# Kernel tuning notes

Measured on AMD Instinct MI355X. Metric: run time of the kernel, lower is better.

The kernel has to match this reference:

```python
import jax, jax.numpy as jnp
import numpy as np

B, NH, T, N, D = 4, 8, 2048, 512, 128
THETA = 2.0 ** 16
GAMMA = 0.995


def setup_inputs() -> dict:
    key = jax.random.key(0)
    kq, kv, ks = jax.random.split(key, 3)
    Q = jax.random.normal(kq, (B, NH, T, N), jnp.float32)
    V = jax.random.normal(kv, (B, NH, T, D), jnp.float32)
    S_prev = 0.01 * jax.random.normal(ks, (B, NH, N, D), jnp.float32)
    # get_freqs(N, theta=2**16): per-channel inverse frequencies
    freqs = jnp.asarray(1.0 / THETA ** (np.arange(N, dtype=np.float32) / N), jnp.float32)
    gamma = jnp.float32(GAMMA)
    return {"Q": Q, "V": V, "S_prev": S_prev, "freqs": freqs, "gamma": gamma}


def _rope(phases, v):
    """Rotary embedding with per-channel phases. phases broadcasts against v's
    last two dims (T, N); rotate-half formulation."""
    cos, sin = jnp.cos(phases), jnp.sin(phases)
    half = v.shape[-1] // 2
    v_rot = jnp.concatenate([-v[..., half:], v[..., :half]], axis=-1)
    return v * cos + v_rot * sin


def reference(Q, V, S_prev, freqs, gamma):
    # Q: (B,nh,T,N)  V: (B,nh,T,D)  S_prev: (B,nh,N,D)
    t_len = Q.shape[2]
    phases = jnp.arange(t_len, dtype=freqs.dtype)[:, None] * freqs[None, :]  # (T,N)
    QR = _rope(phases[None, None], Q)  # K == Q per the module's assert

    q_seq = jnp.moveaxis(QR, 2, 0)  # (T,B,nh,N)
    v_seq = jnp.moveaxis(V, 2, 0)   # (T,B,nh,D)

    def step(S, qv):
        q_t, v_t = qv
        out_t = jnp.einsum('bhn,bhnd->bhd', q_t, S)          # read before write
        S_new = (S + jnp.einsum('bhn,bhd->bhnd', q_t, v_t)) * gamma  # write + decay
        return S_new, out_t

    S_final, outs = jax.lax.scan(step, S_prev, (q_seq, v_seq))
    output = jnp.moveaxis(outs, 0, 2)  # (B,nh,T,D)
    return output, S_final
```

## Files before the change

kernel.cpp:

```cpp
#include <hip/hip_runtime.h>
#include <hip/hip_bf16.h>

typedef __attribute__((ext_vector_type(8))) short short8;
typedef __attribute__((ext_vector_type(4))) short short4v;
typedef __attribute__((ext_vector_type(4))) float f32x4;

#define MFMA16(a,b,c) __builtin_amdgcn_mfma_f32_16x16x32_bf16((a),(b),(c),0,0,0)

constexpr int BHn = 32;
constexpr int Tn  = 2048;
constexpr int Nn  = 512;
constexpr int Dn  = 128;
constexpr int CHn = 64;
constexpr int NCH = Tn / CHn;

static __device__ __forceinline__ unsigned short f2b(float x){
  __hip_bfloat16 h = __float2bfloat16(x);
  return *reinterpret_cast<unsigned short*>(&h);
}

__global__ __launch_bounds__(256) void rope_k(const float* __restrict__ Q,
                                              const float* __restrict__ freqs,
                                              unsigned short* __restrict__ QRq){
  int tq  = blockIdx.x & 511;
  int bh0 = (blockIdx.x >> 9) << 3;
  int np  = threadIdx.x;
  float f1 = freqs[np], f2 = freqs[np + 256];
  float s1[4], c1[4], s2[4], c2[4];
  #pragma unroll
  for (int i = 0; i < 4; ++i){
    float tf = (float)(tq * 4 + i);
    sincosf(tf * f1, &s1[i], &c1[i]);
    sincosf(tf * f2, &s2[i], &c2[i]);
  }
  for (int b = 0; b < 8; ++b){
    int bh = bh0 + b;
    const float* qp = Q + (size_t)bh * Tn * Nn + (size_t)(tq * 4) * Nn + np;
    short4v o1, o2;
    #pragma unroll
    for (int i = 0; i < 4; ++i){
      float q1 = qp[(size_t)i * Nn], q2 = qp[(size_t)i * Nn + 256];
      o1[i] = (short)f2b(q1 * c1[i] - q2 * s1[i]);
      o2[i] = (short)f2b(q2 * c2[i] + q1 * s2[i]);
    }
    unsigned short* dst = QRq + (size_t)bh * Tn * Nn + (size_t)tq * 2048;
    *reinterpret_cast<short4v*>(dst + np * 4)         = o1;
    *reinterpret_cast<short4v*>(dst + (np + 256) * 4) = o2;
  }
}

__device__ __forceinline__ short8 ldfrag(const unsigned short* buf, int rowbase, int k0, int ld, int lane){
  int row = rowbase + (lane & 15);
  int col = (k0 + ((lane >> 4) << 3)) ^ ((row & 7) << 3);
  return *reinterpret_cast<const short8*>(buf + row * ld + col);
}

__device__ __forceinline__ void stage_q(unsigned short* Rs, uint4 v, int dt0, int n0){
  unsigned w0 = v.x, w1 = v.y, w2 = v.z, w3 = v.w;
  unsigned o0 = (w0 & 0xffffu) | (w2 << 16);
  unsigned o1 = (w0 >> 16)     | (w2 & 0xffff0000u);
  unsigned o2 = (w1 & 0xffffu) | (w3 << 16);
  unsigned o3 = (w1 >> 16)     | (w3 & 0xffff0000u);
  *reinterpret_cast<unsigned*>(&Rs[(dt0    ) * 512 + (n0 ^ (((dt0    ) & 7) << 3))]) = o0;
  *reinterpret_cast<unsigned*>(&Rs[(dt0 + 1) * 512 + (n0 ^ (((dt0 + 1) & 7) << 3))]) = o1;
  *reinterpret_cast<unsigned*>(&Rs[(dt0 + 2) * 512 + (n0 ^ (((dt0 + 2) & 7) << 3))]) = o2;
  *reinterpret_cast<unsigned*>(&Rs[(dt0 + 3) * 512 + (n0 ^ (((dt0 + 3) & 7) << 3))]) = o3;
}

__global__ __launch_bounds__(512, 1) void lattn_main(
    const unsigned short* __restrict__ QRq,
    const float* __restrict__ V,
    const float* __restrict__ S_prev,
    const float* __restrict__ gammap,
    float* __restrict__ Out,
    float* __restrict__ Sfin)
{
  __shared__ __align__(16) unsigned short Rs [64 * 512];
  __shared__ __align__(16) unsigned short SbTs[16 * 512];
  __shared__ __align__(16) unsigned short VTs[2][16 * 64];
  __shared__ __align__(16) unsigned short Ps [64 * 64];
  __shared__ float gpow[65], gpinv[65];

  const int tid  = threadIdx.x;
  const int w    = tid >> 6;
  const int lane = tid & 63;
  const int bh   = blockIdx.x & 31;
  const int dch  = blockIdx.x >> 5;
  const int d0   = dch * 16;
  const float g  = gammap[0];

  const unsigned short* QRbh = QRq + (size_t)bh * Tn * Nn;
  const float* Vbh = V + (size_t)bh * Tn * Dn;

  if (tid < 65){
    gpow[tid]  = powf(g,  (float)tid);
    gpinv[tid] = powf(g, -(float)tid);
  }
  #pragma unroll
  for (int i = tid; i < 64 * 64; i += 512) Ps[i] = 0;

  f32x4 st[8];
  if (w >= 4){
    int r0 = (w - 4) * 8;
    #pragma unroll
    for (int j = 0; j < 8; ++j){
      int n = (r0 + j) * 16 + (lane & 15);
      const float* sp = S_prev + (size_t)bh * Nn * Dn + (size_t)n * Dn + d0 + ((lane >> 4) << 2);
      st[j] = *reinterpret_cast<const f32x4*>(sp);
    }
  }
  __syncthreads();
  const float g64 = gpow[64];

  {
    #pragma unroll
    for (int i = 0; i < 8; ++i){
      int p = tid + i * 512;
      int tql = p >> 8, n0 = (p & 255) << 1;
      uint4 v = *reinterpret_cast<const uint4*>(QRbh + (size_t)tql * 2048 + n0 * 4);
      stage_q(Rs, v, tql << 2, n0);
    }
    {
      int dtv = tid >> 3, dp = (tid & 7) << 1;
      const float* vp = Vbh + (size_t)dtv * Dn + d0 + dp;
      float sc = gpinv[dtv];
      VTs[0][ dp      * 64 + (dtv ^ (( dp      & 7) << 3))] = f2b(vp[0] * sc);
      VTs[0][(dp + 1) * 64 + (dtv ^ (((dp + 1) & 7) << 3))] = f2b(vp[1] * sc);
    }
    if (w >= 4){
      int r0 = (w - 4) * 8;
      #pragma unroll
      for (int j = 0; j < 8; ++j){
        int n  = (r0 + j) * 16 + (lane & 15);
        int dl = (lane >> 4) << 2;
        #pragma unroll
        for (int r = 0; r < 4; ++r){
          int d = dl + r;
          SbTs[d * 512 + (n ^ ((d & 7) << 3))] = f2b(st[j][r]);
        }
      }
    }
  }
  __syncthreads();

  for (int c = 0; c < NCH; ++c){
    const int t0 = c * CHn;
    const int vb = c & 1;
    const bool pf = (c + 1 < NCH);
    const unsigned short* Qc = QRbh + (size_t)t0 * Nn;

    uint4 rq[8];
    float va0 = 0.f, va1 = 0.f;
    const int dtv_ = tid >> 3;
    if (pf){
      const unsigned short* QRc = QRbh + (size_t)(t0 + CHn) * Nn;
      #pragma unroll
      for (int i = 0; i < 8; ++i){
        int p = tid + i * 512;
        int tql = p >> 8, n0 = (p & 255) << 1;
        rq[i] = *reinterpret_cast<const uint4*>(QRc + (size_t)tql * 2048 + n0 * 4);
      }
      const float* vp = Vbh + (size_t)(t0 + CHn + dtv_) * Dn + d0 + ((tid & 7) << 1);
      va0 = vp[0]; va1 = vp[1];
    }

    f32x4 oacc = {0.f, 0.f, 0.f, 0.f};
    if (w < 4){
      f32x4 p0 = {0.f,0.f,0.f,0.f}, p1 = p0, p2 = p0;
      for (int kb = 0; kb < 16; ++kb){
        int k0 = kb * 32;
        short8 fs = ldfrag(SbTs, 0, k0, 512, lane);
        if (w == 0){
          short8 f0 = ldfrag(Rs,  0, k0, 512, lane);
          short8 f1 = ldfrag(Rs, 16, k0, 512, lane);
          p0   = MFMA16(f0, f0, p0);
          p1   = MFMA16(f1, f0, p1);
          p2   = MFMA16(f1, f1, p2);
          oacc = MFMA16(fs, f0, oacc);
        } else if (w == 1){
          short8 f0 = ldfrag(Rs,  0, k0, 512, lane);
          short8 f1 = ldfrag(Rs, 16, k0, 512, lane);
          short8 f2 = ldfrag(Rs, 32, k0, 512, lane);
          p0   = MFMA16(f2, f0, p0);
          p1   = MFMA16(f2, f1, p1);
          p2   = MFMA16(f2, f2, p2);
          oacc = MFMA16(fs, f2, oacc);
        } else if (w == 2){
          short8 f0 = ldfrag(Rs,  0, k0, 512, lane);
          short8 f1 = ldfrag(Rs, 16, k0, 512, lane);
          short8 f3 = ldfrag(Rs, 48, k0, 512, lane);
          p0   = MFMA16(f3, f0, p0);
          p1   = MFMA16(f3, f1, p1);
          oacc = MFMA16(fs, f3, oacc);
        } else {
          short8 f1 = ldfrag(Rs, 16, k0, 512, lane);
          short8 f2 = ldfrag(Rs, 32, k0, 512, lane);
          short8 f3 = ldfrag(Rs, 48, k0, 512, lane);
          p0   = MFMA16(f3, f2, p0);
          p1   = MFMA16(f3, f3, p1);
          oacc = MFMA16(fs, f1, oacc);
        }
      }
      int tI[3], tJ[3], nt;
      if      (w == 0){ tI[0]=0; tJ[0]=0; tI[1]=1; tJ[1]=0; tI[2]=1; tJ[2]=1; nt = 3; }
      else if (w == 1){ tI[0]=2; tJ[0]=0; tI[1]=2; tJ[1]=1; tI[2]=2; tJ[2]=2; nt = 3; }
      else if (w == 2){ tI[0]=3; tJ[0]=0; tI[1]=3; tJ[1]=1; tI[2]=0; tJ[2]=0; nt = 2; }
      else            { tI[0]=3; tJ[0]=2; tI[1]=3; tJ[1]=3; tI[2]=0; tJ[2]=0; nt = 2; }
      f32x4 pacc[3] = {p0, p1, p2};
      for (int q = 0; q < nt; ++q){
        int j  = tJ[q] * 16 + (lane & 15);
        int i0 = tI[q] * 16 + ((lane >> 4) << 2);
        #pragma unroll
        for (int r = 0; r < 4; ++r){
          int i = i0 + r;
          float v = (j < i) ? pacc[q][r] * gpow[i] : 0.f;
          Ps[i * 64 + (j ^ ((i & 7) << 3))] = f2b(v);
        }
      }
    } else {
      int r0 = (w - 4) * 8;
      #pragma unroll
      for (int ks = 0; ks < 2; ++ks){
        short8 av = ldfrag(VTs[vb], 0, ks * 32, 64, lane);
        #pragma unroll
        for (int j = 0; j < 8; ++j){
          int n   = (r0 + j) * 16 + (lane & 15);
          int dt0 = ks * 32 + ((lane >> 4) << 3);
          const unsigned short* bp = Qc + (size_t)(dt0 >> 2) * 2048 + n * 4;
          short4v lo = *reinterpret_cast<const short4v*>(bp);
          short4v hi = *reinterpret_cast<const short4v*>(bp + 2048);
          short8 bn = __builtin_shufflevector(lo, hi, 0, 1, 2, 3, 4, 5, 6, 7);
          st[j] = MFMA16(av, bn, st[j]);
        }
      }
      #pragma unroll
      for (int j = 0; j < 8; ++j)
        #pragma unroll
        for (int r = 0; r < 4; ++r) st[j][r] *= g64;
    }
    __syncthreads();

    if (w >= 4){
      int r0 = (w - 4) * 8;
      #pragma unroll
      for (int j = 0; j < 8; ++j){
        int n  = (r0 + j) * 16 + (lane & 15);
        int dl = (lane >> 4) << 2;
        #pragma unroll
        for (int r = 0; r < 4; ++r){
          int d = dl + r;
          SbTs[d * 512 + (n ^ ((d & 7) << 3))] = f2b(st[j][r]);
        }
      }
    } else {
      const int itl = (w == 0) ? 0 : (w == 1) ? 2 : (w == 2) ? 3 : 1;
      float gi = gpow[itl * 16 + (lane & 15)];
      #pragma unroll
      for (int r = 0; r < 4; ++r) oacc[r] *= gi;
      #pragma unroll
      for (int ks = 0; ks < 2; ++ks){
        short8 av = ldfrag(VTs[vb], 0, ks * 32, 64, lane);
        short8 bp = ldfrag(Ps, itl * 16, ks * 32, 64, lane);
        oacc = MFMA16(av, bp, oacc);
      }
      int ti = t0 + itl * 16 + (lane & 15);
      float* op = Out + (size_t)bh * Tn * Dn + (size_t)ti * Dn + d0 + ((lane >> 4) << 2);
      *reinterpret_cast<f32x4*>(op) = oacc;
    }
    if (pf){
      #pragma unroll
      for (int i = 0; i < 8; ++i){
        int p = tid + i * 512;
        int tql = p >> 8, n0 = (p & 255) << 1;
        stage_q(Rs, rq[i], tql << 2, n0);
      }
      int dp = (tid & 7) << 1;
      float sc = gpinv[dtv_];
      VTs[vb ^ 1][ dp      * 64 + (dtv_ ^ (( dp      & 7) << 3))] = f2b(va0 * sc);
      VTs[vb ^ 1][(dp + 1) * 64 + (dtv_ ^ (((dp + 1) & 7) << 3))] = f2b(va1 * sc);
    }
    __syncthreads();
  }

  if (w >= 4){
    int r0 = (w - 4) * 8;
    #pragma unroll
    for (int j = 0; j < 8; ++j){
      int n = (r0 + j) * 16 + (lane & 15);
      float* sp = Sfin + (size_t)bh * Nn * Dn + (size_t)n * Dn + d0 + ((lane >> 4) << 2);
      *reinterpret_cast<f32x4*>(sp) = st[j];
    }
  }
}

extern "C" void kernel_launch(void* const* d_in, const int* in_sizes, int n_in,
                              void* d_out, int out_size, void* d_ws, size_t ws_size,
                              hipStream_t stream){
  const float* Q      = (const float*)d_in[0];
  const float* V      = (const float*)d_in[1];
  const float* S_prev = (const float*)d_in[2];
  const float* freqs  = (const float*)d_in[3];
  const float* gamma  = (const float*)d_in[4];
  float* Out  = (float*)d_out;
  float* Sfin = Out + (size_t)BHn * Tn * Dn;
  unsigned short* QRq = (unsigned short*)d_ws;

  rope_k<<<2048, 256, 0, stream>>>(Q, freqs, QRq);
  lattn_main<<<256, 512, 0, stream>>>(QRq, V, S_prev, gamma, Out, Sfin);
}
```

Before: 203.2 us.

## Move inter-chunk output to state waves and defer intra-chunk finish one chunk

The inter-chunk product of the state with the rotated queries is moved from the four P-computing waves to the four state-update waves. The final combine of the decayed inter term with V times P is deferred to the next chunk iteration, using a double-buffered P and the previous V buffer. This aims to balance work between the two wave groups and remove the post-barrier output phase from the P waves. The cost is an extra P buffer in shared memory and a longer critical path for the state waves, which now do the state update, the inter output and the deferred combine.

```diff
diff --git a/kernel.cpp b/kernel.cpp
--- a/kernel.cpp
+++ b/kernel.cpp
@@ -78,7 +78,7 @@
   __shared__ __align__(16) unsigned short Rs [64 * 512];
   __shared__ __align__(16) unsigned short SbTs[16 * 512];
   __shared__ __align__(16) unsigned short VTs[2][16 * 64];
-  __shared__ __align__(16) unsigned short Ps [64 * 64];
+  __shared__ __align__(16) unsigned short Ps [2][64 * 64];
   __shared__ float gpow[65], gpinv[65];
 
   const int tid  = threadIdx.x;
@@ -97,11 +97,12 @@
     gpinv[tid] = powf(g, -(float)tid);
   }
   #pragma unroll
-  for (int i = tid; i < 64 * 64; i += 512) Ps[i] = 0;
+  for (int i = tid; i < 2 * 64 * 64; i += 512){ Ps[0][i] = 0; }
 
   f32x4 st[8];
+  const int itl = w - 4;
   if (w >= 4){
-    int r0 = (w - 4) * 8;
+    int r0 = itl * 8;
     #pragma unroll
     for (int j = 0; j < 8; ++j){
       int n = (r0 + j) * 16 + (lane & 15);
@@ -128,7 +129,7 @@
       VTs[0][(dp + 1) * 64 + (dtv ^ (((dp + 1) & 7) << 3))] = f2b(vp[1] * sc);
     }
     if (w >= 4){
-      int r0 = (w - 4) * 8;
+      int r0 = itl * 8;
       #pragma unroll
       for (int j = 0; j < 8; ++j){
         int n  = (r0 + j) * 16 + (lane & 15);
@@ -143,9 +144,11 @@
   }
   __syncthreads();
 
+  f32x4 oacc_p = {0.f, 0.f, 0.f, 0.f};
+
   for (int c = 0; c < NCH; ++c){
     const int t0 = c * CHn;
-    const int vb = c & 1;
+    const int q  = c & 1;
     const bool pf = (c + 1 < NCH);
     const unsigned short* Qc = QRbh + (size_t)t0 * Nn;
 
@@ -164,64 +167,74 @@
       va0 = vp[0]; va1 = vp[1];
     }
 
-    f32x4 oacc = {0.f, 0.f, 0.f, 0.f};
     if (w < 4){
       f32x4 p0 = {0.f,0.f,0.f,0.f}, p1 = p0, p2 = p0;
       for (int kb = 0; kb < 16; ++kb){
         int k0 = kb * 32;
-        short8 fs = ldfrag(SbTs, 0, k0, 512, lane);
         if (w == 0){
           short8 f0 = ldfrag(Rs,  0, k0, 512, lane);
           short8 f1 = ldfrag(Rs, 16, k0, 512, lane);
-          p0   = MFMA16(f0, f0, p0);
-          p1   = MFMA16(f1, f0, p1);
-          p2   = MFMA16(f1, f1, p2);
-          oacc = MFMA16(fs, f0, oacc);
+          p0 = MFMA16(f0, f0, p0);
+          p1 = MFMA16(f1, f0, p1);
+          p2 = MFMA16(f1, f1, p2);
         } else if (w == 1){
           short8 f0 = ldfrag(Rs,  0, k0, 512, lane);
           short8 f1 = ldfrag(Rs, 16, k0, 512, lane);
           short8 f2 = ldfrag(Rs, 32, k0, 512, lane);
-          p0   = MFMA16(f2, f0, p0);
-          p1   = MFMA16(f2, f1, p1);
-          p2   = MFMA16(f2, f2, p2);
-          oacc = MFMA16(fs, f2, oacc);
+          p0 = MFMA16(f2, f0, p0);
+          p1 = MFMA16(f2, f1, p1);
+          p2 = MFMA16(f2, f2, p2);
         } else if (w == 2){
           short8 f0 = ldfrag(Rs,  0, k0, 512, lane);
           short8 f1 = ldfrag(Rs, 16, k0, 512, lane);
           short8 f3 = ldfrag(Rs, 48, k0, 512, lane);
-          p0   = MFMA16(f3, f0, p0);
-          p1   = MFMA16(f3, f1, p1);
-          oacc = MFMA16(fs, f3, oacc);
+          p0 = MFMA16(f3, f0, p0);
+          p1 = MFMA16(f3, f1, p1);
         } else {
-          short8 f1 = ldfrag(Rs, 16, k0, 512, lane);
           short8 f2 = ldfrag(Rs, 32, k0, 512, lane);
           short8 f3 = ldfrag(Rs, 48, k0, 512, lane);
-          p0   = MFMA16(f3, f2, p0);
-          p1   = MFMA16(f3, f3, p1);
-          oacc = MFMA16(fs, f1, oacc);
-        }
-      }
+          p0 = MFMA16(f3, f2, p0);
+          p1 = MFMA16(f3, f3, p1);
+        }
+      }
+      unsigned short* Pq = &Ps[q][0];
       int tI[3], tJ[3], nt;
       if      (w == 0){ tI[0]=0; tJ[0]=0; tI[1]=1; tJ[1]=0; tI[2]=1; tJ[2]=1; nt = 3; }
       else if (w == 1){ tI[0]=2; tJ[0]=0; tI[1]=2; tJ[1]=1; tI[2]=2; tJ[2]=2; nt = 3; }
       else if (w == 2){ tI[0]=3; tJ[0]=0; tI[1]=3; tJ[1]=1; tI[2]=0; tJ[2]=0; nt = 2; }
       else            { tI[0]=3; tJ[0]=2; tI[1]=3; tJ[1]=3; tI[2]=0; tJ[2]=0; nt = 2; }
       f32x4 pacc[3] = {p0, p1, p2};
-      for (int q = 0; q < nt; ++q){
-        int j  = tJ[q] * 16 + (lane & 15);
-        int i0 = tI[q] * 16 + ((lane >> 4) << 2);
+      for (int z = 0; z < nt; ++z){
+        int j  = tJ[z] * 16 + (lane & 15);
+        int i0 = tI[z] * 16 + ((lane >> 4) << 2);
         #pragma unroll
         for (int r = 0; r < 4; ++r){
           int i = i0 + r;
-          float v = (j < i) ? pacc[q][r] * gpow[i] : 0.f;
-          Ps[i * 64 + (j ^ ((i & 7) << 3))] = f2b(v);
+          float v = (j < i) ? pacc[z][r] * gpow[i] : 0.f;
+          Pq[i * 64 + (j ^ ((i & 7) << 3))] = f2b(v);
         }
       }
     } else {
-      int r0 = (w - 4) * 8;
+      if (c > 0){
+        const int qp = q ^ 1;
+        float gi = gpow[itl * 16 + (lane & 15)];
+        f32x4 o = oacc_p;
+        #pragma unroll
+        for (int r = 0; r < 4; ++r) o[r] *= gi;
+        #pragma unroll
+        for (int ks = 0; ks < 2; ++ks){
+          short8 av = ldfrag(VTs[qp], 0, ks * 32, 64, lane);
+          short8 bp = ldfrag(&Ps[qp][0], itl * 16, ks * 32, 64, lane);
+          o = MFMA16(av, bp, o);
+        }
+        int ti = (t0 - CHn) + itl * 16 + (lane & 15);
+        float* op = Out + (size_t)bh * Tn * Dn + (size_t)ti * Dn + d0 + ((lane >> 4) << 2);
+        *reinterpret_cast<f32x4*>(op) = o;
+      }
+      int r0 = itl * 8;
       #pragma unroll
       for (int ks = 0; ks < 2; ++ks){
-        short8 av = ldfrag(VTs[vb], 0, ks * 32, 64, lane);
+        short8 av = ldfrag(VTs[q], 0, ks * 32, 64, lane);
         #pragma unroll
         for (int j = 0; j < 8; ++j){
           int n   = (r0 + j) * 16 + (lane & 15);
@@ -237,11 +250,19 @@
       for (int j = 0; j < 8; ++j)
         #pragma unroll
         for (int r = 0; r < 4; ++r) st[j][r] *= g64;
+      f32x4 oc = {0.f, 0.f, 0.f, 0.f};
+      for (int kb = 0; kb < 16; ++kb){
+        int k0 = kb * 32;
+        short8 fs = ldfrag(SbTs, 0, k0, 512, lane);
+        short8 fi = ldfrag(Rs, itl * 16, k0, 512, lane);
+        oc = MFMA16(fs, fi, oc);
+      }
+      oacc_p = oc;
     }
     __syncthreads();
 
     if (w >= 4){
-      int r0 = (w - 4) * 8;
+      int r0 = itl * 8;
       #pragma unroll
       for (int j = 0; j < 8; ++j){
         int n  = (r0 + j) * 16 + (lane & 15);
@@ -252,20 +273,6 @@
           SbTs[d * 512 + (n ^ ((d & 7) << 3))] = f2b(st[j][r]);
         }
       }
-    } else {
-      const int itl = (w == 0) ? 0 : (w == 1) ? 2 : (w == 2) ? 3 : 1;
-      float gi = gpow[itl * 16 + (lane & 15)];
-      #pragma unroll
-      for (int r = 0; r < 4; ++r) oacc[r] *= gi;
-      #pragma unroll
-      for (int ks = 0; ks < 2; ++ks){
-        short8 av = ldfrag(VTs[vb], 0, ks * 32, 64, lane);
-        short8 bp = ldfrag(Ps, itl * 16, ks * 32, 64, lane);
-        oacc = MFMA16(av, bp, oacc);
-      }
-      int ti = t0 + itl * 16 + (lane & 15);
-      float* op = Out + (size_t)bh * Tn * Dn + (size_t)ti * Dn + d0 + ((lane >> 4) << 2);
-      *reinterpret_cast<f32x4*>(op) = oacc;
     }
     if (pf){
       #pragma unroll
@@ -276,14 +283,29 @@
       }
       int dp = (tid & 7) << 1;
       float sc = gpinv[dtv_];
-      VTs[vb ^ 1][ dp      * 64 + (dtv_ ^ (( dp      & 7) << 3))] = f2b(va0 * sc);
-      VTs[vb ^ 1][(dp + 1) * 64 + (dtv_ ^ (((dp + 1) & 7) << 3))] = f2b(va1 * sc);
+      VTs[q ^ 1][ dp      * 64 + (dtv_ ^ (( dp      & 7) << 3))] = f2b(va0 * sc);
+      VTs[q ^ 1][(dp + 1) * 64 + (dtv_ ^ (((dp + 1) & 7) << 3))] = f2b(va1 * sc);
     }
     __syncthreads();
   }
 
   if (w >= 4){
-    int r0 = (w - 4) * 8;
+    const int qp = (NCH - 1) & 1;
+    float gi = gpow[itl * 16 + (lane & 15)];
+    f32x4 o = oacc_p;
+    #pragma unroll
+    for (int r = 0; r < 4; ++r) o[r] *= gi;
+    #pragma unroll
+    for (int ks = 0; ks < 2; ++ks){
+      short8 av = ldfrag(VTs[qp], 0, ks * 32, 64, lane);
+      short8 bp = ldfrag(&Ps[qp][0], itl * 16, ks * 32, 64, lane);
+      o = MFMA16(av, bp, o);
+    }
+    int ti = (NCH - 1) * CHn + itl * 16 + (lane & 15);
+    float* op = Out + (size_t)bh * Tn * Dn + (size_t)ti * Dn + d0 + ((lane >> 4) << 2);
+    *reinterpret_cast<f32x4*>(op) = o;
+
+    int r0 = itl * 8;
     #pragma unroll
     for (int j = 0; j < 8; ++j){
       int n = (r0 + j) * 16 + (lane & 15);
```

Measured after the change: 205.3 us. No clear change (+1.0%).
